# Performance work log

Measured on AMD Instinct MI355X. Metric: run time of the kernel, lower is better.

Reference implementation:

```python
import jax
jax.config.update("jax_enable_x64", True)
import jax.numpy as jnp
import numpy as np

# --- Field setup -------------------------------------------------------------
# The original uses BLS12-381 Fr (255-bit Montgomery limbs). JAX has no native
# 256-bit ints, so the reference uses an NTT-friendly 31-bit prime with the
# same algorithmic structure (two-adic radix-2 INTT, grand products, MSM-style
# commitment reduction). Products of two residues fit in int64.
P = 2013265921          # 15 * 2^27 + 1, two-adicity 27
G = 31                  # generator of F_P^*
LOG_N = 20
N = 1 << LOG_N
W = pow(G, (P - 1) // N, P)      # primitive N-th root of unity
W_INV = pow(W, P - 2, P)
N_INV = pow(N, P - 2, P)
K1, K2, K3 = 7, 13, 17           # PLONK coset shifts for wire identities


def _bitrev_perm(n):
    logn = n.bit_length() - 1
    idx = np.arange(n, dtype=np.int64)
    rev = np.zeros(n, dtype=np.int64)
    for i in range(logn):
        rev = (rev << 1) | ((idx >> i) & 1)
    return rev


def _twiddles(n, root):
    logn = n.bit_length() - 1
    out = []
    for s in range(1, logn + 1):
        m = 1 << s
        wm = pow(root, n // m, P)
        half = m >> 1
        ws = np.empty(half, dtype=np.int64)
        w = 1
        for k in range(half):
            ws[k] = w
            w = (w * wm) % P
        out.append(jnp.asarray(ws))
    return out

_BREV = jnp.asarray(_bitrev_perm(N))
_TW_INV = _twiddles(N, W_INV)


def _ntt_core(a, tw):
    # iterative radix-2 Cooley-Tukey, fully vectorized per stage
    n = a.shape[0]
    a = a[_BREV]
    for s, ws in enumerate(tw):
        half = 1 << s
        a = a.reshape(-1, 2 * half)         # [n/(2*half), 2*half]
        u = a[:, :half]
        t = (a[:, half:] * ws[None, :]) % P
        a = jnp.concatenate([(u + t) % P, (u - t) % P], axis=1)
    return a.reshape(n)


def intt(evals):
    # inverse NTT: evaluations on the domain -> coefficients (nn.Intt)
    return (_ntt_core(evals, _TW_INV) * N_INV) % P


def inv_mod(x):
    # batch modular inverse: x^(P-2), exponent is a compile-time constant
    e = P - 2
    res = jnp.ones_like(x)
    base = x % P
    while e:
        if e & 1:
            res = (res * base) % P
        base = (base * base) % P
        e >>= 1
    return res


def cumprod_mod(x):
    return jax.lax.associative_scan(lambda a, b: (a * b) % P, x)


def shifted_cumprod(r):
    # z[0] = 1, z[i] = prod_{j<i} r[j]
    c = cumprod_mod(r)
    return jnp.concatenate([jnp.ones((1,), r.dtype), c[:-1]])


def commit(poly, ck):
    # stand-in for the KZG MSM: <poly, ck> mod P (same reduction structure)
    return jnp.sum((poly * ck) % P) % P


def perm_z(wires, sigmas, beta, gamma, omega_pows):
    # PLONK copy-constraint grand product (mod.compute_permutation_poly)
    ids = (omega_pows, (K1 * omega_pows) % P,
           (K2 * omega_pows) % P, (K3 * omega_pows) % P)
    num = jnp.ones((N,), jnp.int64)
    den = jnp.ones((N,), jnp.int64)
    for w, i, s in zip(wires, ids, sigmas):
        num = (num * ((w + (beta * i) % P + gamma) % P)) % P
        den = (den * ((w + (beta * s) % P + gamma) % P)) % P
    return shifted_cumprod((num * inv_mod(den)) % P)


def lookup_z2(f, t, h1, h2, delta, epsilon):
    # plookup grand product (mod.compute_lookup_permutation_poly)
    one_plus_d = (1 + delta) % P
    ep1d = (epsilon * one_plus_d) % P
    t_next = jnp.roll(t, -1)
    h1_next = jnp.roll(h1, -1)
    h2_next = jnp.roll(h2, -1)
    num = (one_plus_d * ((epsilon + f) % P)) % P
    num = (num * ((ep1d + t + (delta * t_next) % P) % P)) % P
    a = (ep1d + h1 + (delta * h1_next) % P) % P
    b = (ep1d + h2 + (delta * h2_next) % P) % P
    den = (a * b) % P
    return shifted_cumprod((num * inv_mod(den)) % P)


def setup_inputs() -> dict:
    key = jax.random.key(0)
    ks = jax.random.split(key, 16)
    def ri(k):
        return jax.random.randint(k, (N,), 0, P, dtype=jnp.int64)
    return {
        "w_l": ri(ks[0]), "w_r": ri(ks[1]), "w_o": ri(ks[2]), "w_4": ri(ks[3]),
        "q_lookup": jax.random.randint(ks[4], (N,), 0, 2, dtype=jnp.int64),
        "t1": ri(ks[5]), "t2": ri(ks[6]), "t3": ri(ks[7]), "t4": ri(ks[8]),
        "sigma_l": ri(ks[9]), "sigma_r": ri(ks[10]),
        "sigma_o": ri(ks[11]), "sigma_4": ri(ks[12]),
        "ck": ri(ks[13]),
        "zeta": 123457, "beta": 98765, "gamma": 54321,
        "delta": 13579, "epsilon": 24680,
    }


def reference(w_l, w_r, w_o, w_4, q_lookup, t1, t2, t3, t4,
              sigma_l, sigma_r, sigma_o, sigma_4, ck,
              zeta, beta, gamma, delta, epsilon):
    z2c = (zeta * zeta) % P
    z3c = (z2c * zeta) % P
    # zkp.compress: zeta-combine lookup table columns
    t = (t1 + (zeta * t2) % P + (z2c * t3) % P + (z3c * t4) % P) % P
    table_poly = intt(t)
    # zkp.compute_query_table: compressed wire query where selector is on,
    # padded with table values where it is off
    q = (w_l + (zeta * w_r) % P + (z2c * w_o) % P + (z3c * w_4) % P) % P
    f = jnp.where(q_lookup == 1, q, t)
    f_poly = intt(f)
    # witness INTTs
    w_l_poly = intt(w_l)
    w_r_poly = intt(w_r)
    w_o_poly = intt(w_o)
    w_4_poly = intt(w_4)
    # combine_split: sorted multiset of f union t, split alternating
    s = jnp.sort(jnp.concatenate([f, t]))
    h1, h2 = s[0::2], s[1::2]
    h1_poly = intt(h1)
    h2_poly = intt(h2)
    # domain elements 1, W, W^2, ...
    omega_pows = shifted_cumprod(jnp.full((N,), W, dtype=jnp.int64))
    z = perm_z((w_l, w_r, w_o, w_4), (sigma_l, sigma_r, sigma_o, sigma_4),
               beta, gamma, omega_pows)
    z_poly = intt(z)
    z2 = lookup_z2(f, t, h1, h2, delta, epsilon)
    z2_poly = intt(z2)
    polys = (w_l_poly, w_r_poly, w_o_poly, w_4_poly, f_poly, table_poly,
             h1_poly, h2_poly, z_poly, z2_poly)
    commits = jnp.stack([commit(p, ck) for p in polys])
    return polys + (commits,)
```

## Files before the change

### kernel.cpp

```cpp
#include <hip/hip_runtime.h>
#include <stdint.h>

#define PRIME 2013265921u
#define LOGN  20
#define NN    (1u << LOGN)

static constexpr uint64_t cpowmod(uint64_t b, uint64_t e){
  uint64_t r = 1; b %= PRIME;
  while (e){ if (e & 1) r = r * b % PRIME; b = b * b % PRIME; e >>= 1; }
  return r;
}
static constexpr uint32_t WFWD = (uint32_t)cpowmod(31u, (PRIME - 1u) >> LOGN);
static constexpr uint32_t WINV = (uint32_t)cpowmod(WFWD, PRIME - 2u);
static constexpr uint32_t NINV = (uint32_t)cpowmod(NN, PRIME - 2u);
static constexpr uint64_t MBAR = 0xFFFFFFFFFFFFFFFFull / PRIME;

__device__ uint32_t g_U[1024];
__device__ uint32_t g_V[1024];
__device__ uint2    g_TWp[1024];
__device__ uint2    g_U2p[1024];
__device__ uint32_t g_bcnt[2048];
__device__ uint32_t g_boff[2048];
__device__ uint32_t g_bcur[2048];
__device__ uint32_t g_btot[2048];
__device__ uint32_t g_bpre[2048];
__device__ unsigned long long g_commit[10];

__device__ __forceinline__ uint32_t mulmod(uint32_t a, uint32_t b){
  uint64_t t = (uint64_t)a * b;
  uint32_t q = (uint32_t)__umul64hi(t, MBAR);
  uint32_t r = (uint32_t)t - q * PRIME;
  if (r >= PRIME) r -= PRIME;
  return r;
}
__device__ __forceinline__ uint32_t shoup_mul(uint32_t a, uint32_t w, uint32_t ws){
  uint32_t q = __umulhi(a, ws);
  uint32_t r = a * w - q * PRIME;
  if (r >= PRIME) r -= PRIME;
  return r;
}
__device__ __forceinline__ uint32_t addmod(uint32_t a, uint32_t b){
  uint32_t s = a + b; return (s >= PRIME) ? s - PRIME : s;
}
__device__ __forceinline__ uint32_t submod(uint32_t a, uint32_t b){
  return (a >= b) ? (a - b) : (a + (PRIME - b));
}
__device__ __forceinline__ uint32_t addmod3(uint32_t a, uint32_t b, uint32_t c){
  return addmod(addmod(a, b), c);
}
__device__ __forceinline__ uint32_t powmod_dev(uint32_t b, uint32_t e){
  uint32_t r = 1u;
  while (e){ if (e & 1u) r = mulmod(r, b); b = mulmod(b, b); e >>= 1u; }
  return r;
}

__global__ __launch_bounds__(1024) void k_zero(){
  const uint32_t t = blockIdx.x * 1024u + threadIdx.x;
  if (t < 2048u) g_bcnt[t] = 0u;
  if (t < 10u)   g_commit[t] = 0ull;
}

__global__ __launch_bounds__(1024) void k_tables(){
  const uint32_t i = threadIdx.x;
  if (blockIdx.x == 0){
    g_U[i] = powmod_dev(WINV, i);
  } else if (blockIdx.x == 1){
    g_V[i] = powmod_dev(WINV, i << 10);
  } else if (blockIdx.x == 2){
    const uint32_t w = mulmod(NINV, powmod_dev(WINV, i));
    g_U2p[i] = make_uint2(w, (uint32_t)((((uint64_t)w) << 32) / PRIME));
  } else {
    uint32_t j;
    if      (i < 512u)  j = i;
    else if (i < 768u)  j = (i - 512u)  << 1;
    else if (i < 896u)  j = (i - 768u)  << 2;
    else if (i < 960u)  j = (i - 896u)  << 3;
    else if (i < 992u)  j = (i - 960u)  << 4;
    else if (i < 1008u) j = (i - 992u)  << 5;
    else if (i < 1016u) j = (i - 1008u) << 6;
    else if (i < 1020u) j = (i - 1016u) << 7;
    else if (i < 1022u) j = (i - 1020u) << 8;
    else                j = 0u;
    const uint32_t w = powmod_dev(WINV, j << 10);
    g_TWp[i] = make_uint2(w, (uint32_t)((((uint64_t)w) << 32) / PRIME));
  }
}

__global__ __launch_bounds__(1024) void k_elemA(
    const uint32_t* __restrict__ wl, const uint32_t* __restrict__ wr,
    const uint32_t* __restrict__ wo, const uint32_t* __restrict__ w4,
    const uint32_t* __restrict__ ql, const uint32_t* __restrict__ x1,
    const uint32_t* __restrict__ x2, const uint32_t* __restrict__ x3,
    const uint32_t* __restrict__ x4, const uint32_t* __restrict__ zeta_p,
    uint32_t* __restrict__ o32)
{
  __shared__ uint32_t hcnt[2048];
  const int t = threadIdx.x;
  hcnt[t] = 0u; hcnt[t + 1024] = 0u;
  __syncthreads();

  const uint32_t zeta = zeta_p[0];
  const uint32_t zc2 = mulmod(zeta, zeta), zc3 = mulmod(zc2, zeta);
  const uint32_t i0 = (uint32_t)blockIdx.x * 4096u + (uint32_t)t * 4u;

  uint4 vt1 = *(const uint4*)(x1 + i0);
  uint4 vt2 = *(const uint4*)(x2 + i0);
  uint4 vt3 = *(const uint4*)(x3 + i0);
  uint4 vt4 = *(const uint4*)(x4 + i0);
  uint4 vwl = *(const uint4*)(wl + i0);
  uint4 vwr = *(const uint4*)(wr + i0);
  uint4 vwo = *(const uint4*)(wo + i0);
  uint4 vw4 = *(const uint4*)(w4 + i0);
  uint4 vql = *(const uint4*)(ql + i0);

  uint32_t T1[4] = {vt1.x, vt1.y, vt1.z, vt1.w};
  uint32_t T2[4] = {vt2.x, vt2.y, vt2.z, vt2.w};
  uint32_t T3[4] = {vt3.x, vt3.y, vt3.z, vt3.w};
  uint32_t T4[4] = {vt4.x, vt4.y, vt4.z, vt4.w};
  uint32_t L1[4] = {vwl.x, vwl.y, vwl.z, vwl.w};
  uint32_t L2[4] = {vwr.x, vwr.y, vwr.z, vwr.w};
  uint32_t L3[4] = {vwo.x, vwo.y, vwo.z, vwo.w};
  uint32_t L4[4] = {vw4.x, vw4.y, vw4.z, vw4.w};
  uint32_t QL[4] = {vql.x, vql.y, vql.z, vql.w};

  uint32_t tv[4], fv[4];
  #pragma unroll
  for (int k = 0; k < 4; ++k){
    uint32_t tt = addmod(addmod(T1[k], mulmod(zeta, T2[k])),
                         addmod(mulmod(zc2, T3[k]), mulmod(zc3, T4[k])));
    uint32_t qq = addmod(addmod(L1[k], mulmod(zeta, L2[k])),
                         addmod(mulmod(zc2, L3[k]), mulmod(zc3, L4[k])));
    tv[k] = tt; fv[k] = (QL[k] == 1u) ? qq : tt;
  }
  uint4 o;
  o.x = tv[0]; o.y = tv[1]; o.z = tv[2]; o.w = tv[3];
  *(uint4*)(o32 + 5u*NN + i0) = o;
  o.x = fv[0]; o.y = fv[1]; o.z = fv[2]; o.w = fv[3];
  *(uint4*)(o32 + 4u*NN + i0) = o;

  #pragma unroll
  for (int k = 0; k < 4; ++k){ atomicAdd(&hcnt[fv[k] >> 20], 1u);
                               atomicAdd(&hcnt[tv[k] >> 20], 1u); }
  __syncthreads();
  uint32_t c0 = hcnt[t];          if (c0) atomicAdd(&g_bcnt[t], c0);
  uint32_t c1 = hcnt[t + 1024];   if (c1) atomicAdd(&g_bcnt[t + 1024], c1);
}

__global__ __launch_bounds__(1024) void k_bscan(){
  __shared__ uint32_t SA[2048], SB[2048];
  const int t = threadIdx.x;
  SA[t] = g_bcnt[t];
  SA[t + 1024] = g_bcnt[t + 1024];
  __syncthreads();
  uint32_t* sp = SA; uint32_t* dp = SB;
  for (int off = 1; off < 2048; off <<= 1){
    for (int i = t; i < 2048; i += 1024)
      dp[i] = (i >= off) ? (sp[i - off] + sp[i]) : sp[i];
    uint32_t* tmp = sp; sp = dp; dp = tmp;
    __syncthreads();
  }
  uint32_t e0 = t ? sp[t - 1] : 0u;
  uint32_t e1 = sp[t + 1023];
  g_boff[t] = e0;         g_bcur[t] = e0;
  g_boff[t + 1024] = e1;  g_bcur[t + 1024] = e1;
}

__global__ __launch_bounds__(1024) void k_scat2(uint32_t* __restrict__ o32){
  __shared__ uint32_t sorted[8192];
  __shared__ uint32_t hist[2048];
  __shared__ uint32_t SA[2048];
  __shared__ uint32_t wsum[16];
  __shared__ uint32_t gbase[2048];
  const int t = threadIdx.x;
  const uint32_t base = blockIdx.x * 8192u;

  hist[t] = 0u; hist[t + 1024] = 0u;
  __syncthreads();

  uint32_t v[8], rk[8];
  #pragma unroll
  for (int k = 0; k < 8; ++k)
    v[k] = o32[4u*NN + base + (uint32_t)t + (uint32_t)k * 1024u];
  #pragma unroll
  for (int k = 0; k < 8; ++k)
    rk[k] = atomicAdd(&hist[v[k] >> 20], 1u);
  __syncthreads();

  const uint32_t lane = (uint32_t)t & 63u, wid = (uint32_t)t >> 6;
  const uint32_t e0 = hist[2*t], e1 = hist[2*t + 1];
  const uint32_t s = e0 + e1;
  uint32_t scan = s;
  #pragma unroll
  for (int off = 1; off < 64; off <<= 1){
    uint32_t u = __shfl_up(scan, off, 64);
    if (lane >= (uint32_t)off) scan += u;
  }
  if (lane == 63u) wsum[wid] = scan;
  __syncthreads();
  if (t < 64){
    uint32_t u = (t < 16) ? wsum[t] : 0u;
    #pragma unroll
    for (int off = 1; off < 16; off <<= 1){
      uint32_t x2 = __shfl_up(u, off, 64);
      if ((uint32_t)t >= (uint32_t)off) u += x2;
    }
    if (t < 16) wsum[t] = u;
  }
  __syncthreads();
  const uint32_t wbase = wid ? wsum[wid - 1] : 0u;
  const uint32_t incl = wbase + scan;
  SA[2*t]     = incl - e1;
  SA[2*t + 1] = incl;
  __syncthreads();
  uint32_t* sp = SA;

  for (int b = t; b < 2048; b += 1024){
    uint32_t c = hist[b];
    if (c) gbase[b] = atomicAdd(&g_bcur[b], c);
  }
  __syncthreads();

  #pragma unroll
  for (int k = 0; k < 8; ++k){
    uint32_t b = v[k] >> 20;
    uint32_t ls = b ? sp[b - 1] : 0u;
    sorted[ls + rk[k]] = v[k];
  }
  __syncthreads();

  for (int i = t; i < 8192; i += 1024){
    uint32_t vv = sorted[i];
    uint32_t b = vv >> 20;
    uint32_t ls = b ? sp[b - 1] : 0u;
    o32[6u*NN + gbase[b] + (uint32_t)i - ls] = vv;
  }
}

__global__ __launch_bounds__(256) void k_bsort(uint32_t* __restrict__ o32){
  __shared__ uint32_t sorted[2048];
  __shared__ uint32_t SA[1024], SB[1024];
  __shared__ uint32_t wsum[4];
  const int b = blockIdx.x, t = threadIdx.x;
  uint32_t n = g_bcnt[b]; if (n > 2048u) n = 2048u;
  const uint32_t off = g_boff[b];

  for (int i = t; i < 1024; i += 256) SA[i] = 0u;
  __syncthreads();

  uint32_t v[8], rk[8];
  #pragma unroll
  for (int k = 0; k < 8; ++k){
    const uint32_t i = (uint32_t)t + (uint32_t)k * 256u;
    if (i < n){
      v[k] = o32[6u*NN + off + i];
      rk[k] = atomicAdd(&SA[(v[k] >> 10) & 1023u], 1u);
    }
  }
  __syncthreads();

  const uint32_t lane = (uint32_t)t & 63u, wid = (uint32_t)t >> 6;
  const uint32_t h0 = SA[4*t], h1 = SA[4*t + 1], h2 = SA[4*t + 2], h3 = SA[4*t + 3];
  const uint32_t s = h0 + h1 + h2 + h3;
  uint32_t scan = s;
  #pragma unroll
  for (int o = 1; o < 64; o <<= 1){
    uint32_t u = __shfl_up(scan, o, 64);
    if (lane >= (uint32_t)o) scan += u;
  }
  if (lane == 63u) wsum[wid] = scan;
  __syncthreads();
  if (t < 64){
    uint32_t u = (t < 4) ? wsum[t] : 0u;
    #pragma unroll
    for (int o = 1; o < 4; o <<= 1){
      uint32_t x2 = __shfl_up(u, o, 64);
      if ((uint32_t)t >= (uint32_t)o) u += x2;
    }
    if (t < 4) wsum[t] = u;
  }
  __syncthreads();
  const uint32_t wbase = wid ? wsum[wid - 1] : 0u;
  const uint32_t incl = wbase + scan;
  SB[4*t + 3] = incl;
  SB[4*t + 2] = incl - h3;
  SB[4*t + 1] = incl - h3 - h2;
  SB[4*t + 0] = incl - h3 - h2 - h1;
  __syncthreads();
  uint32_t* sp = SB;

  #pragma unroll
  for (int k = 0; k < 8; ++k){
    const uint32_t i = (uint32_t)t + (uint32_t)k * 256u;
    if (i < n){
      const uint32_t d = (v[k] >> 10) & 1023u;
      const uint32_t s2 = d ? sp[d - 1] : 0u;
      sorted[s2 + rk[k]] = v[k];
    }
  }
  __syncthreads();

  for (int d = t; d < 1024; d += 256){
    const uint32_t s2 = d ? sp[d - 1] : 0u;
    const uint32_t e = sp[d];
    for (uint32_t i = s2 + 1; i < e; ++i){
      const uint32_t key = sorted[i];
      uint32_t j = i;
      while (j > s2 && sorted[j - 1] > key){ sorted[j] = sorted[j - 1]; --j; }
      sorted[j] = key;
    }
  }
  __syncthreads();

  for (uint32_t i = (uint32_t)t; i < n; i += 256u) o32[6u*NN + off + i] = sorted[i];
}

__global__ __launch_bounds__(256) void k_ratio(
    const uint32_t* __restrict__ wl, const uint32_t* __restrict__ wr,
    const uint32_t* __restrict__ wo, const uint32_t* __restrict__ w4,
    const uint32_t* __restrict__ sl, const uint32_t* __restrict__ sr,
    const uint32_t* __restrict__ so, const uint32_t* __restrict__ s4,
    const uint32_t* __restrict__ beta_p, const uint32_t* __restrict__ gamma_p,
    const uint32_t* __restrict__ delta_p, const uint32_t* __restrict__ eps_p,
    uint32_t* __restrict__ o32)
{
  __shared__ uint32_t SA[256], SB[256];
  const int blk = blockIdx.x, t = threadIdx.x;
  const int second = blk >> 9;
  const uint32_t base = ((uint32_t)(blk & 511) << 11) + ((uint32_t)t << 3);
  uint32_t num[8], den[8];
  if (!second){
    const uint32_t beta = beta_p[0], gamma = gamma_p[0];
    #pragma unroll
    for (int k = 0; k < 8; ++k){
      uint32_t i = base + (uint32_t)k;
      uint32_t e = (NN - i) & (NN - 1u);
      uint32_t om = mulmod(g_U[e & 1023u], g_V[e >> 10]);
      uint32_t bo = mulmod(beta, om);
      uint32_t n = addmod3(wl[i], bo, gamma);
      n = mulmod(n, addmod3(wr[i], mulmod(7u,  bo), gamma));
      n = mulmod(n, addmod3(wo[i], mulmod(13u, bo), gamma));
      n = mulmod(n, addmod3(w4[i], mulmod(17u, bo), gamma));
      uint32_t d = addmod3(wl[i], mulmod(beta, sl[i]), gamma);
      d = mulmod(d, addmod3(wr[i], mulmod(beta, sr[i]), gamma));
      d = mulmod(d, addmod3(wo[i], mulmod(beta, so[i]), gamma));
      d = mulmod(d, addmod3(w4[i], mulmod(beta, s4[i]), gamma));
      num[k] = n; den[k] = d;
    }
  } else {
    const uint32_t del = delta_p[0], ep = eps_p[0];
    const uint32_t opd = addmod(1u, del), ep1d = mulmod(ep, opd);
    #pragma unroll
    for (int k = 0; k < 8; ++k){
      uint32_t i = base + (uint32_t)k;
      uint32_t fi = o32[4u*NN + i], ti = o32[5u*NN + i];
      uint32_t tn = o32[5u*NN + ((i + 1u) & (NN - 1u))];
      uint32_t h1  = o32[6u*NN + 2u*i];
      uint32_t h2  = o32[6u*NN + 2u*i + 1u];
      uint32_t h1n = o32[6u*NN + ((2u*i + 2u) & (2u*NN - 1u))];
      uint32_t h2n = o32[6u*NN + ((2u*i + 3u) & (2u*NN - 1u))];
      uint32_t n = mulmod(opd, addmod(ep, fi));
      n = mulmod(n, addmod3(ep1d, ti, mulmod(del, tn)));
      uint32_t d = mulmod(addmod3(ep1d, h1, mulmod(del, h1n)),
                          addmod3(ep1d, h2, mulmod(del, h2n)));
      num[k] = n; den[k] = d;
    }
  }
  bool ok = true;
  #pragma unroll
  for (int k = 0; k < 8; ++k) ok = ok && (den[k] != 0u);
  uint32_t r[8];
  if (ok){
    uint32_t pp[8];
    pp[0] = den[0];
    #pragma unroll
    for (int k = 1; k < 8; ++k) pp[k] = mulmod(pp[k-1], den[k]);
    uint32_t iv = powmod_dev(pp[7], PRIME - 2u);
    #pragma unroll
    for (int k = 7; k >= 1; --k){
      r[k] = mulmod(num[k], mulmod(iv, pp[k-1]));
      iv = mulmod(iv, den[k]);
    }
    r[0] = mulmod(num[0], iv);
  } else {
    #pragma unroll
    for (int k = 0; k < 8; ++k) r[k] = mulmod(num[k], powmod_dev(den[k], PRIME - 2u));
  }
  uint32_t tp = r[0];
  #pragma unroll
  for (int k = 1; k < 8; ++k) tp = mulmod(tp, r[k]);
  SA[t] = tp; __syncthreads();
  uint32_t* sp = SA; uint32_t* dp = SB;
  for (int off = 1; off < 256; off <<= 1){
    dp[t] = (t >= off) ? mulmod(sp[t - off], sp[t]) : sp[t];
    uint32_t* tmp = sp; sp = dp; dp = tmp;
    __syncthreads();
  }
  if (t == 255) g_btot[blk] = sp[255];
  uint32_t run = t ? sp[t - 1] : 1u;
  const uint32_t zo = 8u*NN + ((uint32_t)second << 20) + base;
  #pragma unroll
  for (int k = 0; k < 8; ++k){
    o32[zo + (uint32_t)k] = run;
    run = mulmod(run, r[k]);
  }
}

__global__ __launch_bounds__(512) void k_btscan(){
  __shared__ uint32_t SA[512], SB[512];
  const int a = blockIdx.x, t = threadIdx.x;
  SA[t] = g_btot[a * 512 + t];
  __syncthreads();
  uint32_t* sp = SA; uint32_t* dp = SB;
  for (int off = 1; off < 512; off <<= 1){
    dp[t] = (t >= off) ? mulmod(sp[t - off], sp[t]) : sp[t];
    uint32_t* tmp = sp; sp = dp; dp = tmp;
    __syncthreads();
  }
  g_bpre[a * 512 + t] = t ? sp[t - 1] : 1u;
}

__global__ __launch_bounds__(256) void k_apply(uint32_t* __restrict__ o32){
  const uint32_t g = blockIdx.x * 256u + threadIdx.x;
  const uint32_t base = g << 2;
  const uint32_t m = g_bpre[base >> 11];
  uint4* zz = (uint4*)(o32 + 8u*NN);
  uint4 v = zz[g];
  v.x = mulmod(v.x, m); v.y = mulmod(v.y, m); v.z = mulmod(v.z, m); v.w = mulmod(v.w, m);
  zz[g] = v;
}

struct Desc  { const uint32_t* p; uint32_t stride; uint32_t off; };
struct Descs { Desc d[10]; };
struct Map   { int g[10]; };

#define SWZ8(i, c) (((i) << 3) + ((c) ^ (((i) >> 2) & 7)))

__device__ __forceinline__ void ntt1024_reg(uint32_t x[16], int l,
                                            const uint2* __restrict__ sTW){
  #pragma unroll
  for (int st = 9; st >= 6; --st){
    const int bb = 1 << (st - 6);
    const int base = (st == 9) ? 0 : (st == 8) ? 512 : (st == 7) ? 768 : 896;
    #pragma unroll
    for (int r = 0; r < 16; ++r){
      if ((r & bb) == 0){
        const int r2 = r | bb;
        const uint32_t u = x[r], v = x[r2];
        const uint2 wv = sTW[base + ((r & (bb - 1)) << 6) + l];
        x[r]  = addmod(u, v);
        x[r2] = shoup_mul(submod(u, v), wv.x, wv.y);
      }
    }
  }
  #pragma unroll
  for (int st = 5; st >= 0; --st){
    const int h = 1 << st;
    const int base = (st == 5) ? 960 : (st == 4) ? 992 : (st == 3) ? 1008
                   : (st == 2) ? 1016 : (st == 1) ? 1020 : 1022;
    const uint2 wv = sTW[base + (l & (h - 1))];
    const bool hi = (l & h) != 0;
    #pragma unroll
    for (int r = 0; r < 16; ++r){
      const uint32_t y = __shfl_xor(x[r], h, 64);
      const uint32_t a = addmod(x[r], y);
      const uint32_t b = shoup_mul(submod(y, x[r]), wv.x, wv.y);
      x[r] = hi ? b : a;
    }
  }
}

__global__ __launch_bounds__(512, 8) void k_intt1(Descs ds, uint32_t* __restrict__ mid){
  __shared__ uint32_t tile[8192];
  __shared__ uint2 sTW[1024];
  const int t = threadIdx.x;
  sTW[t] = g_TWp[t];
  sTW[t + 512] = g_TWp[t + 512];
  const int arr = blockIdx.x >> 6;
  const Desc de = ds.d[arr];
  const int w = t >> 6, l = t & 63;
  uint32_t* mo = mid + ((size_t)arr << 20);

  for (int ti = 0; ti < 2; ++ti){
    const int c0 = ((((blockIdx.x & 63) << 1) | ti) << 3);
    if (ti) __syncthreads();
    if (de.stride == 1u){
      #pragma unroll
      for (int it = 0; it < 4; ++it){
        const int row = (it << 8) + (t >> 1);
        const int cb = (t & 1) << 2;
        uint4 v = *(const uint4*)(de.p + (size_t)row * 1024u + (uint32_t)(c0 + cb));
        tile[SWZ8(row, cb + 0)] = v.x; tile[SWZ8(row, cb + 1)] = v.y;
        tile[SWZ8(row, cb + 2)] = v.z; tile[SWZ8(row, cb + 3)] = v.w;
      }
    } else {
      #pragma unroll
      for (int it = 0; it < 4; ++it){
        const int row = (it << 8) + (t >> 1);
        const int cb = (t & 1) << 2;
        const size_t b0 = 2u * ((size_t)row * 1024u + (uint32_t)(c0 + cb));
        uint4 a0 = *(const uint4*)(de.p + b0);
        uint4 a1 = *(const uint4*)(de.p + b0 + 4u);
        if (de.off == 0u){
          tile[SWZ8(row, cb + 0)] = a0.x; tile[SWZ8(row, cb + 1)] = a0.z;
          tile[SWZ8(row, cb + 2)] = a1.x; tile[SWZ8(row, cb + 3)] = a1.z;
        } else {
          tile[SWZ8(row, cb + 0)] = a0.y; tile[SWZ8(row, cb + 1)] = a0.w;
          tile[SWZ8(row, cb + 2)] = a1.y; tile[SWZ8(row, cb + 3)] = a1.w;
        }
      }
    }
    __syncthreads();
    uint32_t x[16];
    #pragma unroll
    for (int r = 0; r < 16; ++r) x[r] = tile[SWZ8(l + (r << 6), w)];
    ntt1024_reg(x, l, sTW);
    const uint32_t i1g = (uint32_t)(c0 + w);
    const uint32_t rl = __brev((uint32_t)l) >> 26;
    #pragma unroll
    for (int r = 0; r < 16; ++r){
      const uint32_t rr = __brev((uint32_t)r) >> 28;
      const uint32_t j1 = (rl << 4) | rr;
      const uint32_t e = j1 * i1g;
      const uint2 wa = g_U2p[e & 1023u];
      const uint32_t hv = e >> 10;
      const uint2 wb = sTW[hv & 511u];
      uint32_t wbw = wb.x, wbs = wb.y;
      if (hv & 512u){ wbw = PRIME - wbw; wbs = ~wbs; }
      x[r] = shoup_mul(x[r], wa.x, wa.y);
      x[r] = shoup_mul(x[r], wbw, wbs);
    }
    #pragma unroll
    for (int r = 0; r < 16; ++r) tile[SWZ8(l + (r << 6), w)] = x[r];
    __syncthreads();
    #pragma unroll
    for (int it = 0; it < 4; ++it){
      const int row = (it << 8) + (t >> 1);
      const int cb = (t & 1) << 2;
      uint4 v;
      v.x = tile[SWZ8(row, cb + 0)]; v.y = tile[SWZ8(row, cb + 1)];
      v.z = tile[SWZ8(row, cb + 2)]; v.w = tile[SWZ8(row, cb + 3)];
      *(uint4*)(mo + (size_t)row * 1024u + (uint32_t)(c0 + cb)) = v;
    }
  }
}

__global__ __launch_bounds__(512, 8) void k_intt2(const uint32_t* __restrict__ mid,
                                                  uint32_t* __restrict__ o32,
                                                  const uint32_t* __restrict__ ck,
                                                  Map mp){
  __shared__ uint32_t tile[8192];
  __shared__ uint2 sTW[1024];
  __shared__ unsigned long long redw[8];
  const int t = threadIdx.x;
  sTW[t] = g_TWp[t];
  sTW[t + 512] = g_TWp[t + 512];
  const int arrL = blockIdx.x >> 6;
  const int gidx = mp.g[arrL];
  const int w = t >> 6, l = t & 63;
  const uint32_t* mi = mid + ((size_t)arrL << 20);
  uint32_t* oa = o32 + ((size_t)gidx << 20);
  unsigned long long acc = 0ull;

  for (int ti = 0; ti < 2; ++ti){
    const int m0 = ((((blockIdx.x & 63) << 1) | ti) << 3);
    if (ti) __syncthreads();
    const uint32_t p = __brev((uint32_t)(m0 + w)) >> 22;
    #pragma unroll
    for (int it = 0; it < 4; ++it){
      const int kb = (it << 8) + (l << 2);
      uint4 v = *(const uint4*)(mi + p * 1024u + (uint32_t)kb);
      tile[SWZ8(kb + 0, w)] = v.x; tile[SWZ8(kb + 1, w)] = v.y;
      tile[SWZ8(kb + 2, w)] = v.z; tile[SWZ8(kb + 3, w)] = v.w;
    }
    __syncthreads();
    uint32_t x[16];
    #pragma unroll
    for (int r = 0; r < 16; ++r) x[r] = tile[SWZ8(l + (r << 6), w)];
    ntt1024_reg(x, l, sTW);
    #pragma unroll
    for (int r = 0; r < 16; ++r) tile[SWZ8(l + (r << 6), w)] = x[r];
    __syncthreads();
    #pragma unroll
    for (int it = 0; it < 4; ++it){
      const int j2 = (it << 8) + (t >> 1);
      const int rb = (t & 1) << 2;
      const uint32_t q = __brev((uint32_t)j2) >> 22;
      uint4 v;
      v.x = tile[SWZ8((int)q, rb + 0)]; v.y = tile[SWZ8((int)q, rb + 1)];
      v.z = tile[SWZ8((int)q, rb + 2)]; v.w = tile[SWZ8((int)q, rb + 3)];
      const uint32_t oi = (uint32_t)j2 * 1024u + (uint32_t)(m0 + rb);
      *(uint4*)(oa + oi) = v;
      uint4 cv = *(const uint4*)(ck + oi);
      acc += (unsigned long long)mulmod(v.x, cv.x);
      acc += (unsigned long long)mulmod(v.y, cv.y);
      acc += (unsigned long long)mulmod(v.z, cv.z);
      acc += (unsigned long long)mulmod(v.w, cv.w);
    }
  }
  #pragma unroll
  for (int off = 32; off >= 1; off >>= 1) acc += __shfl_down(acc, off, 64);
  if (l == 0) redw[w] = acc;
  __syncthreads();
  if (t < 64){
    unsigned long long s = (t < 8) ? redw[t] : 0ull;
    #pragma unroll
    for (int off = 4; off >= 1; off >>= 1) s += __shfl_down(s, off, 64);
    if (t == 0) atomicAdd(&g_commit[gidx], s);
  }
}

__global__ __launch_bounds__(256) void k_brev(const uint32_t* __restrict__ src,
                                              uint32_t stride, uint32_t off,
                                              uint32_t* __restrict__ dst){
  const uint32_t i = blockIdx.x * 256u + threadIdx.x;
  const uint32_t r = __brev(i) >> 12;
  dst[i] = src[(size_t)r * stride + off];
}

__global__ __launch_bounds__(1024) void k_stage09(uint32_t* __restrict__ wk){
  __shared__ uint32_t sm[1024];
  const int t = threadIdx.x;
  const uint32_t gbase = blockIdx.x * 1024u;
  sm[t] = wk[gbase + t];
  __syncthreads();
  for (int s = 0; s <= 9; ++s){
    if (t < 512){
      const int half = 1 << s;
      const int k = t & (half - 1);
      const int i0 = ((t >> s) << (s + 1)) | k;
      const int i1 = i0 + half;
      const uint32_t tw = g_V[(uint32_t)k << (9 - s)];
      const uint32_t u = sm[i0];
      const uint32_t tv = mulmod(sm[i1], tw);
      sm[i0] = addmod(u, tv);
      sm[i1] = submod(u, tv);
    }
    __syncthreads();
  }
  wk[gbase + t] = sm[t];
}

__global__ __launch_bounds__(256) void k_stage(uint32_t* __restrict__ wk, int s){
  const uint32_t q = blockIdx.x * 256u + threadIdx.x;
  const uint32_t half = 1u << s;
  const uint32_t k = q & (half - 1u);
  const uint32_t i0 = ((q >> s) << (s + 1)) | k;
  const uint32_t i1 = i0 + half;
  const uint32_t e = k << (19 - s);
  const uint32_t tw = mulmod(g_U[e & 1023u], g_V[e >> 10]);
  const uint32_t u = wk[i0];
  const uint32_t tv = mulmod(wk[i1], tw);
  wk[i0] = addmod(u, tv);
  wk[i1] = submod(u, tv);
}

__global__ __launch_bounds__(1024) void k_scale_commit(const uint32_t* __restrict__ src,
                                                       uint32_t* dst,
                                                       const uint32_t* __restrict__ ck,
                                                       int cidx){
  __shared__ unsigned long long red[1024];
  const uint32_t i = blockIdx.x * 1024u + threadIdx.x;
  const uint32_t val = mulmod(src[i], NINV);
  dst[i] = val;
  red[threadIdx.x] = (unsigned long long)mulmod(val, ck[i]);
  __syncthreads();
  for (int s = 512; s > 0; s >>= 1){
    if ((int)threadIdx.x < s) red[threadIdx.x] += red[threadIdx.x + s];
    __syncthreads();
  }
  if (threadIdx.x == 0) atomicAdd(&g_commit[cidx], red[0]);
}

__global__ void k_final(uint32_t* __restrict__ out){
  const int i = threadIdx.x;
  if (i < 10) out[(size_t)10 * NN + i] = (uint32_t)(g_commit[i] % (unsigned long long)PRIME);
}

extern "C" void kernel_launch(void* const* d_in, const int* in_sizes, int n_in,
                              void* d_out, int out_size, void* d_ws, size_t ws_size,
                              hipStream_t stream)
{
  const uint32_t* wl   = (const uint32_t*)d_in[0];
  const uint32_t* wr   = (const uint32_t*)d_in[1];
  const uint32_t* wo   = (const uint32_t*)d_in[2];
  const uint32_t* w4   = (const uint32_t*)d_in[3];
  const uint32_t* ql   = (const uint32_t*)d_in[4];
  const uint32_t* t1   = (const uint32_t*)d_in[5];
  const uint32_t* t2   = (const uint32_t*)d_in[6];
  const uint32_t* t3   = (const uint32_t*)d_in[7];
  const uint32_t* t4   = (const uint32_t*)d_in[8];
  const uint32_t* sl   = (const uint32_t*)d_in[9];
  const uint32_t* sr   = (const uint32_t*)d_in[10];
  const uint32_t* so   = (const uint32_t*)d_in[11];
  const uint32_t* s4   = (const uint32_t*)d_in[12];
  const uint32_t* ck   = (const uint32_t*)d_in[13];
  const uint32_t* zeta = (const uint32_t*)d_in[14];
  const uint32_t* beta = (const uint32_t*)d_in[15];
  const uint32_t* gam  = (const uint32_t*)d_in[16];
  const uint32_t* del  = (const uint32_t*)d_in[17];
  const uint32_t* eps  = (const uint32_t*)d_in[18];
  uint32_t* o32 = (uint32_t*)d_out;
  (void)in_sizes; (void)n_in; (void)out_size;

  k_zero  <<<2, 1024, 0, stream>>>();
  k_tables<<<4, 1024, 0, stream>>>();
  k_elemA <<<256, 1024, 0, stream>>>(wl, wr, wo, w4, ql, t1, t2, t3, t4, zeta, o32);
  k_bscan <<<1, 1024, 0, stream>>>();
  k_scat2 <<<256, 1024, 0, stream>>>(o32);
  k_bsort <<<1920, 256, 0, stream>>>(o32);
  k_ratio <<<1024, 256, 0, stream>>>(wl, wr, wo, w4, sl, sr, so, s4, beta, gam, del, eps, o32);
  k_btscan<<<2, 512, 0, stream>>>();
  k_apply <<<2048, 256, 0, stream>>>(o32);

  Desc ds[10];
  ds[0] = { wl,          1u, 0u };
  ds[1] = { wr,          1u, 0u };
  ds[2] = { wo,          1u, 0u };
  ds[3] = { w4,          1u, 0u };
  ds[4] = { o32 + 4u*NN, 1u, 0u };
  ds[5] = { o32 + 5u*NN, 1u, 0u };
  ds[6] = { o32 + 6u*NN, 2u, 0u };
  ds[7] = { o32 + 6u*NN, 2u, 1u };
  ds[8] = { o32 + 8u*NN, 1u, 0u };
  ds[9] = { o32 + 9u*NN, 1u, 0u };

  const size_t wsWords = ws_size / 4u;
  if (wsWords >= 2ull * NN){
    static const int ord[10] = {6,7, 4,5, 8,9, 0,1, 2,3};
    const int chunk = (wsWords >= 10ull * NN) ? 10 : 2;
    uint32_t* mid = (uint32_t*)d_ws;
    for (int s0 = 0; s0 < 10; s0 += chunk){
      const int cnt = (10 - s0 < chunk) ? (10 - s0) : chunk;
      Descs sub; Map mp;
      for (int a = 0; a < 10; ++a){
        const int g = ord[(a < cnt) ? s0 + a : s0];
        sub.d[a] = ds[g]; mp.g[a] = g;
      }
      k_intt1<<<64 * cnt, 512, 0, stream>>>(sub, mid);
      k_intt2<<<64 * cnt, 512, 0, stream>>>(mid, o32, ck, mp);
    }
  } else {
    auto run_intt = [&](const Desc& d, uint32_t workSlot, int dstSlot){
      uint32_t* wk = o32 + (size_t)workSlot * NN;
      k_brev   <<<4096, 256, 0, stream>>>(d.p, d.stride, d.off, wk);
      k_stage09<<<1024, 1024, 0, stream>>>(wk);
      for (int s = 10; s < 20; ++s)
        k_stage<<<2048, 256, 0, stream>>>(wk, s);
      k_scale_commit<<<1024, 1024, 0, stream>>>(wk, o32 + (size_t)dstSlot * NN, ck, dstSlot);
    };
    k_brev<<<4096, 256, 0, stream>>>(ds[6].p, 2u, 0u, o32 + 0u*NN);
    k_brev<<<4096, 256, 0, stream>>>(ds[7].p, 2u, 1u, o32 + 1u*NN);
    {
      uint32_t* wk0 = o32;
      uint32_t* wk1 = o32 + NN;
      k_stage09<<<1024, 1024, 0, stream>>>(wk0);
      for (int s = 10; s < 20; ++s) k_stage<<<2048, 256, 0, stream>>>(wk0, s);
      k_scale_commit<<<1024, 1024, 0, stream>>>(wk0, o32 + 6u*NN, ck, 6);
      k_stage09<<<1024, 1024, 0, stream>>>(wk1);
      for (int s = 10; s < 20; ++s) k_stage<<<2048, 256, 0, stream>>>(wk1, s);
      k_scale_commit<<<1024, 1024, 0, stream>>>(wk1, o32 + 7u*NN, ck, 7);
    }
    run_intt(ds[4], 0u, 4);
    run_intt(ds[5], 1u, 5);
    run_intt(ds[8], 0u, 8);
    run_intt(ds[9], 1u, 9);
    run_intt(ds[0], 0u, 0);
    run_intt(ds[1], 1u, 1);
    run_intt(ds[2], 2u, 2);
    run_intt(ds[3], 3u, 3);
  }
  k_final<<<1, 64, 0, stream>>>(o32);
}
```

Baseline: 232.5 us.

## Use 1024-thread persistent blocks with atomic tile scheduler for four-step INTT

The two column/row INTT passes now run as persistent 1024-thread blocks that pull 16-column tiles from a global atomic work counter, replacing fixed 512-thread blocks that each processed two 8-column tiles. The shared tile doubles to 16K words with a new 16-wide swizzle, and the per-block commit reduction becomes a per-wave atomicAdd per tile. The aim is better load balance and fewer block launches, at the cost of more shared memory per block (lower occupancy), extra atomics, and an added reset kernel launch.

```diff
diff --git a/kernel.cpp b/kernel.cpp
--- a/kernel.cpp
+++ b/kernel.cpp
@@ -24,6 +24,7 @@
 __device__ uint32_t g_bcur[2048];
 __device__ uint32_t g_btot[2048];
 __device__ uint32_t g_bpre[2048];
+__device__ uint32_t g_work[4];
 __device__ unsigned long long g_commit[10];
 
 __device__ __forceinline__ uint32_t mulmod(uint32_t a, uint32_t b){
@@ -58,6 +59,11 @@
   const uint32_t t = blockIdx.x * 1024u + threadIdx.x;
   if (t < 2048u) g_bcnt[t] = 0u;
   if (t < 10u)   g_commit[t] = 0ull;
+  if (t < 4u)    g_work[t] = 0u;
+}
+
+__global__ void k_wrst(){
+  if (threadIdx.x < 4) g_work[threadIdx.x] = 0u;
 }
 
 __global__ __launch_bounds__(1024) void k_tables(){
@@ -433,7 +439,7 @@
 struct Descs { Desc d[10]; };
 struct Map   { int g[10]; };
 
-#define SWZ8(i, c) (((i) << 3) + ((c) ^ (((i) >> 2) & 7)))
+#define SWZ(i, c) (((i) << 4) + ((c) ^ (((i) >> 1) & 15)))
 
 __device__ __forceinline__ void ntt1024_reg(uint32_t x[16], int l,
                                             const uint2* __restrict__ sTW){
@@ -469,50 +475,54 @@
   }
 }
 
-__global__ __launch_bounds__(512, 8) void k_intt1(Descs ds, uint32_t* __restrict__ mid){
-  __shared__ uint32_t tile[8192];
+__global__ __launch_bounds__(1024, 8) void k_intt1(Descs ds, uint32_t* __restrict__ mid,
+                                                   int ntiles){
+  __shared__ uint32_t tile[16384];
   __shared__ uint2 sTW[1024];
+  __shared__ uint32_t s_idx;
   const int t = threadIdx.x;
   sTW[t] = g_TWp[t];
-  sTW[t + 512] = g_TWp[t + 512];
-  const int arr = blockIdx.x >> 6;
-  const Desc de = ds.d[arr];
   const int w = t >> 6, l = t & 63;
-  uint32_t* mo = mid + ((size_t)arr << 20);
-
-  for (int ti = 0; ti < 2; ++ti){
-    const int c0 = ((((blockIdx.x & 63) << 1) | ti) << 3);
-    if (ti) __syncthreads();
+
+  for (;;){
+    if (t == 0) s_idx = atomicAdd(&g_work[0], 1u);
+    __syncthreads();
+    const uint32_t idx = s_idx;
+    if (idx >= (uint32_t)ntiles) break;
+    const int arr = (int)(idx >> 6);
+    const int c0 = (int)(idx & 63u) << 4;
+    const Desc de = ds.d[arr];
+
     if (de.stride == 1u){
       #pragma unroll
       for (int it = 0; it < 4; ++it){
-        const int row = (it << 8) + (t >> 1);
-        const int cb = (t & 1) << 2;
+        const int row = (it << 8) + (t >> 2);
+        const int cb = (t & 3) << 2;
         uint4 v = *(const uint4*)(de.p + (size_t)row * 1024u + (uint32_t)(c0 + cb));
-        tile[SWZ8(row, cb + 0)] = v.x; tile[SWZ8(row, cb + 1)] = v.y;
-        tile[SWZ8(row, cb + 2)] = v.z; tile[SWZ8(row, cb + 3)] = v.w;
+        tile[SWZ(row, cb + 0)] = v.x; tile[SWZ(row, cb + 1)] = v.y;
+        tile[SWZ(row, cb + 2)] = v.z; tile[SWZ(row, cb + 3)] = v.w;
       }
     } else {
       #pragma unroll
       for (int it = 0; it < 4; ++it){
-        const int row = (it << 8) + (t >> 1);
-        const int cb = (t & 1) << 2;
+        const int row = (it << 8) + (t >> 2);
+        const int cb = (t & 3) << 2;
         const size_t b0 = 2u * ((size_t)row * 1024u + (uint32_t)(c0 + cb));
         uint4 a0 = *(const uint4*)(de.p + b0);
         uint4 a1 = *(const uint4*)(de.p + b0 + 4u);
         if (de.off == 0u){
-          tile[SWZ8(row, cb + 0)] = a0.x; tile[SWZ8(row, cb + 1)] = a0.z;
-          tile[SWZ8(row, cb + 2)] = a1.x; tile[SWZ8(row, cb + 3)] = a1.z;
+          tile[SWZ(row, cb + 0)] = a0.x; tile[SWZ(row, cb + 1)] = a0.z;
+          tile[SWZ(row, cb + 2)] = a1.x; tile[SWZ(row, cb + 3)] = a1.z;
         } else {
-          tile[SWZ8(row, cb + 0)] = a0.y; tile[SWZ8(row, cb + 1)] = a0.w;
-          tile[SWZ8(row, cb + 2)] = a1.y; tile[SWZ8(row, cb + 3)] = a1.w;
+          tile[SWZ(row, cb + 0)] = a0.y; tile[SWZ(row, cb + 1)] = a0.w;
+          tile[SWZ(row, cb + 2)] = a1.y; tile[SWZ(row, cb + 3)] = a1.w;
         }
       }
     }
     __syncthreads();
     uint32_t x[16];
     #pragma unroll
-    for (int r = 0; r < 16; ++r) x[r] = tile[SWZ8(l + (r << 6), w)];
+    for (int r = 0; r < 16; ++r) x[r] = tile[SWZ(l + (r << 6), w)];
     ntt1024_reg(x, l, sTW);
     const uint32_t i1g = (uint32_t)(c0 + w);
     const uint32_t rl = __brev((uint32_t)l) >> 26;
@@ -529,65 +539,70 @@
       x[r] = shoup_mul(x[r], wa.x, wa.y);
       x[r] = shoup_mul(x[r], wbw, wbs);
     }
-    #pragma unroll
-    for (int r = 0; r < 16; ++r) tile[SWZ8(l + (r << 6), w)] = x[r];
-    __syncthreads();
+    __syncthreads();
+    #pragma unroll
+    for (int r = 0; r < 16; ++r) tile[SWZ(l + (r << 6), w)] = x[r];
+    __syncthreads();
+    uint32_t* mo = mid + ((size_t)arr << 20);
     #pragma unroll
     for (int it = 0; it < 4; ++it){
-      const int row = (it << 8) + (t >> 1);
-      const int cb = (t & 1) << 2;
+      const int row = (it << 8) + (t >> 2);
+      const int cb = (t & 3) << 2;
       uint4 v;
-      v.x = tile[SWZ8(row, cb + 0)]; v.y = tile[SWZ8(row, cb + 1)];
-      v.z = tile[SWZ8(row, cb + 2)]; v.w = tile[SWZ8(row, cb + 3)];
+      v.x = tile[SWZ(row, cb + 0)]; v.y = tile[SWZ(row, cb + 1)];
+      v.z = tile[SWZ(row, cb + 2)]; v.w = tile[SWZ(row, cb + 3)];
       *(uint4*)(mo + (size_t)row * 1024u + (uint32_t)(c0 + cb)) = v;
     }
   }
 }
 
-__global__ __launch_bounds__(512, 8) void k_intt2(const uint32_t* __restrict__ mid,
-                                                  uint32_t* __restrict__ o32,
-                                                  const uint32_t* __restrict__ ck,
-                                                  Map mp){
-  __shared__ uint32_t tile[8192];
+__global__ __launch_bounds__(1024, 8) void k_intt2(const uint32_t* __restrict__ mid,
+                                                   uint32_t* __restrict__ o32,
+                                                   const uint32_t* __restrict__ ck,
+                                                   Map mp, int ntiles){
+  __shared__ uint32_t tile[16384];
   __shared__ uint2 sTW[1024];
-  __shared__ unsigned long long redw[8];
+  __shared__ uint32_t s_idx;
   const int t = threadIdx.x;
   sTW[t] = g_TWp[t];
-  sTW[t + 512] = g_TWp[t + 512];
-  const int arrL = blockIdx.x >> 6;
-  const int gidx = mp.g[arrL];
   const int w = t >> 6, l = t & 63;
-  const uint32_t* mi = mid + ((size_t)arrL << 20);
-  uint32_t* oa = o32 + ((size_t)gidx << 20);
-  unsigned long long acc = 0ull;
-
-  for (int ti = 0; ti < 2; ++ti){
-    const int m0 = ((((blockIdx.x & 63) << 1) | ti) << 3);
-    if (ti) __syncthreads();
+
+  for (;;){
+    if (t == 0) s_idx = atomicAdd(&g_work[1], 1u);
+    __syncthreads();
+    const uint32_t idx = s_idx;
+    if (idx >= (uint32_t)ntiles) break;
+    const int arrL = (int)(idx >> 6);
+    const int m0 = (int)(idx & 63u) << 4;
+    const int gidx = mp.g[arrL];
+    const uint32_t* mi = mid + ((size_t)arrL << 20);
     const uint32_t p = __brev((uint32_t)(m0 + w)) >> 22;
     #pragma unroll
     for (int it = 0; it < 4; ++it){
       const int kb = (it << 8) + (l << 2);
       uint4 v = *(const uint4*)(mi + p * 1024u + (uint32_t)kb);
-      tile[SWZ8(kb + 0, w)] = v.x; tile[SWZ8(kb + 1, w)] = v.y;
-      tile[SWZ8(kb + 2, w)] = v.z; tile[SWZ8(kb + 3, w)] = v.w;
+      tile[SWZ(kb + 0, w)] = v.x; tile[SWZ(kb + 1, w)] = v.y;
+      tile[SWZ(kb + 2, w)] = v.z; tile[SWZ(kb + 3, w)] = v.w;
     }
     __syncthreads();
     uint32_t x[16];
     #pragma unroll
-    for (int r = 0; r < 16; ++r) x[r] = tile[SWZ8(l + (r << 6), w)];
+    for (int r = 0; r < 16; ++r) x[r] = tile[SWZ(l + (r << 6), w)];
     ntt1024_reg(x, l, sTW);
-    #pragma unroll
-    for (int r = 0; r < 16; ++r) tile[SWZ8(l + (r << 6), w)] = x[r];
-    __syncthreads();
+    __syncthreads();
+    #pragma unroll
+    for (int r = 0; r < 16; ++r) tile[SWZ(l + (r << 6), w)] = x[r];
+    __syncthreads();
+    unsigned long long acc = 0ull;
+    uint32_t* oa = o32 + ((size_t)gidx << 20);
     #pragma unroll
     for (int it = 0; it < 4; ++it){
-      const int j2 = (it << 8) + (t >> 1);
-      const int rb = (t & 1) << 2;
+      const int j2 = (it << 8) + (t >> 2);
+      const int rb = (t & 3) << 2;
       const uint32_t q = __brev((uint32_t)j2) >> 22;
       uint4 v;
-      v.x = tile[SWZ8((int)q, rb + 0)]; v.y = tile[SWZ8((int)q, rb + 1)];
-      v.z = tile[SWZ8((int)q, rb + 2)]; v.w = tile[SWZ8((int)q, rb + 3)];
+      v.x = tile[SWZ((int)q, rb + 0)]; v.y = tile[SWZ((int)q, rb + 1)];
+      v.z = tile[SWZ((int)q, rb + 2)]; v.w = tile[SWZ((int)q, rb + 3)];
       const uint32_t oi = (uint32_t)j2 * 1024u + (uint32_t)(m0 + rb);
       *(uint4*)(oa + oi) = v;
       uint4 cv = *(const uint4*)(ck + oi);
@@ -596,16 +611,10 @@
       acc += (unsigned long long)mulmod(v.z, cv.z);
       acc += (unsigned long long)mulmod(v.w, cv.w);
     }
-  }
-  #pragma unroll
-  for (int off = 32; off >= 1; off >>= 1) acc += __shfl_down(acc, off, 64);
-  if (l == 0) redw[w] = acc;
-  __syncthreads();
-  if (t < 64){
-    unsigned long long s = (t < 8) ? redw[t] : 0ull;
-    #pragma unroll
-    for (int off = 4; off >= 1; off >>= 1) s += __shfl_down(s, off, 64);
-    if (t == 0) atomicAdd(&g_commit[gidx], s);
+    #pragma unroll
+    for (int off = 32; off >= 1; off >>= 1) acc += __shfl_down(acc, off, 64);
+    if (l == 0) atomicAdd(&g_commit[gidx], acc);
+    __syncthreads();
   }
 }
 
@@ -736,8 +745,11 @@
         const int g = ord[(a < cnt) ? s0 + a : s0];
         sub.d[a] = ds[g]; mp.g[a] = g;
       }
-      k_intt1<<<64 * cnt, 512, 0, stream>>>(sub, mid);
-      k_intt2<<<64 * cnt, 512, 0, stream>>>(mid, o32, ck, mp);
+      const int ntiles = 64 * cnt;
+      const int grid = (ntiles < 512) ? ntiles : 512;
+      k_wrst <<<1, 64, 0, stream>>>();
+      k_intt1<<<grid, 1024, 0, stream>>>(sub, mid, ntiles);
+      k_intt2<<<grid, 1024, 0, stream>>>(mid, o32, ck, mp, ntiles);
     }
   } else {
     auto run_intt = [&](const Desc& d, uint32_t workSlot, int dstSlot){
```

After: 305.3 us. +31.3%, slower.
